# Kernel optimization log

Hardware: AMD Instinct MI355X
Metric: run time of the kernel (lower is better)

Reference implementation:

```python
import jax, jax.numpy as jnp
import numpy as np
from jax import lax

D = 1024  # inputSize == hidden size
B = 128   # batch
T = 256   # step


def setup_inputs() -> dict:
    key = jax.random.key(0)
    ks = jax.random.split(key, 9)
    s = 1.0 / np.sqrt(D)  # torch LSTMCell/Linear default init scale
    return {
        "inp": jax.random.normal(ks[0], (B, T, D), dtype=jnp.float32),
        "h0": jnp.zeros((B, D), dtype=jnp.float32),
        "c0": jnp.zeros((B, D), dtype=jnp.float32),
        "W_ih": jax.random.uniform(ks[1], (4 * D, D), jnp.float32, -s, s),
        "W_hh": jax.random.uniform(ks[2], (4 * D, D), jnp.float32, -s, s),
        "b_ih": jax.random.uniform(ks[3], (4 * D,), jnp.float32, -s, s),
        "b_hh": jax.random.uniform(ks[4], (4 * D,), jnp.float32, -s, s),
        "fc_w": jax.random.uniform(ks[5], (1, D), jnp.float32, -s, s),
        "fc_b": jax.random.uniform(ks[6], (1,), jnp.float32, -s, s),
        "step": T,
    }


def reference(inp, h0, c0, W_ih, W_hh, b_ih, b_hh, fc_w, fc_b, step):
    # The original's double python loop just transposes [B, T, D] -> [T, B, D].
    xs = jnp.swapaxes(inp, 0, 1)  # [T, B, D]

    def cell(carry, x):
        h, c = carry
        # torch.nn.LSTMCell gate order: i, f, g, o
        gates = x @ W_ih.T + b_ih + h @ W_hh.T + b_hh  # [B, 4D]
        i, f, g, o = jnp.split(gates, 4, axis=-1)
        i = jax.nn.sigmoid(i)
        f = jax.nn.sigmoid(f)
        g = jnp.tanh(g)
        o = jax.nn.sigmoid(o)
        c2 = f * c + i * g
        h2 = o * jnp.tanh(c2)
        return (h2, c2), None

    (hx, cx), _ = lax.scan(cell, (h0, c0), xs)
    yhat = jax.nn.sigmoid(hx @ fc_w.T + fc_b)  # [B, 1]
    return (yhat, hx, cx)
```

## Files before the change

### kernel.cpp

```cpp
#include <hip/hip_runtime.h>
#include <hip/hip_cooperative_groups.h>

namespace cg = cooperative_groups;

#define Dd 1024
#define Bb 128
#define Tt 256
#define NWG 256
#define NTHR 256

typedef short bf16x8 __attribute__((ext_vector_type(8)));
typedef float f32x4 __attribute__((ext_vector_type(4)));
typedef unsigned long long u64;

static __device__ __forceinline__ unsigned short f2bf(float x) {
  unsigned int u = __float_as_uint(x);
  u += 0x7fffu + ((u >> 16) & 1u);
  return (unsigned short)(u >> 16);
}
static __device__ __forceinline__ unsigned int pk2(float a, float b) {
  return (unsigned int)f2bf(a) | ((unsigned int)f2bf(b) << 16);
}
static __device__ __forceinline__ bf16x8 as_bf(uint4 u) {
  union { uint4 u; bf16x8 v; } x; x.u = u; return x.v;
}
static __device__ __forceinline__ f32x4 mfma_(bf16x8 a, bf16x8 b, f32x4 c) {
  return __builtin_amdgcn_mfma_f32_16x16x32_bf16(a, b, c, 0, 0, 0);
}
static __device__ __forceinline__ float sigm(float x) { return 1.f / (1.f + __expf(-x)); }
static __device__ __forceinline__ float tanh_s(float x) { return 1.f - 2.f / (__expf(2.f * x) + 1.f); }
static __device__ __forceinline__ u64 aload(const u64* p) {
  return __hip_atomic_load(p, __ATOMIC_RELAXED, __HIP_MEMORY_SCOPE_AGENT);
}
static __device__ __forceinline__ void astore(u64* p, u64 v) {
  __hip_atomic_store(p, v, __ATOMIC_RELAXED, __HIP_MEMORY_SCOPE_AGENT);
}

__global__ void __launch_bounds__(NTHR, 1) lstm_kernel(
    const float* __restrict__ inp, const float* __restrict__ h0,
    const float* __restrict__ c0, const float* __restrict__ W_ih,
    const float* __restrict__ W_hh, const float* __restrict__ b_ih,
    const float* __restrict__ b_hh, const float* __restrict__ fc_w,
    const float* __restrict__ fc_b, float* __restrict__ out,
    int* __restrict__ flags, unsigned short* __restrict__ hbuf,
    unsigned short* __restrict__ xbf, int use_xbf)
{
  extern __shared__ uint4 ldsW[];
  __shared__ float red[4];

  const int tid = threadIdx.x;
  const int wg  = blockIdx.x;
  const int gid = wg * NTHR + tid;
  cg::grid_group grid = cg::this_grid();

  const int gs = wg >> 1;
  const int bh = wg & 1;

  if (tid < 4)
    __hip_atomic_store(&flags[bh * 512 + gs * 4 + tid], 0,
                       __ATOMIC_RELAXED, __HIP_MEMORY_SCOPE_AGENT);

  if (use_xbf) {
    for (int i = gid; i < Tt * Bb * (Dd / 8); i += NWG * NTHR) {
      int d8 = i & 127, b = (i >> 7) & 127, t = i >> 14;
      const float* s = inp + ((size_t)b * Tt + t) * Dd + d8 * 8;
      uint4 p;
      p.x = pk2(s[0], s[1]); p.y = pk2(s[2], s[3]);
      p.z = pk2(s[4], s[5]); p.w = pk2(s[6], s[7]);
      *(uint4*)(xbf + (size_t)i * 8) = p;
    }
  }
  uint4* hb4w = (uint4*)hbuf;
  for (int i = gid; i < 128 * 128; i += NWG * NTHR) {
    int row = i & 127, gsl = i >> 7;
    const float* s = h0 + (size_t)row * Dd + gsl * 8;
    uint4 p;
    p.x = pk2(s[0], s[1]); p.y = pk2(s[2], s[3]);
    p.z = pk2(s[4], s[5]); p.w = pk2(s[6], s[7]);
    hb4w[gsl * 128 + row] = p;
  }

  for (int i = tid; i < 8192; i += NTHR) {
    int l2 = i & 63, mmct = (i >> 6) & 3, kc = i >> 8;
    int cc = l2 & 15, ct = mmct & 1;
    int row = (((ct << 1) | (cc >> 3)) << 10) | (gs << 3) | (cc & 7);
    int k = kc * 32 + ((l2 >> 4) << 3);
    const float* s = ((mmct & 2) ? W_hh : W_ih) + (size_t)row * Dd + k;
    uint4 p;
    p.x = pk2(s[0], s[1]); p.y = pk2(s[2], s[3]);
    p.z = pk2(s[4], s[5]); p.w = pk2(s[6], s[7]);
    ldsW[i] = p;
  }

  const int w = tid >> 6, l = tid & 63;
  const int c = l & 15;
  const int rowbase = bh * 64 + w * 16;
  const int arow = rowbase + c;
  const int koff8 = l >> 4;
  const int r0 = ((c >> 3) << 10) | (gs << 3) | (c & 7);
  const int r1 = ((2 + (c >> 3)) << 10) | (gs << 3) | (c & 7);
  const float bias0 = b_ih[r0] + b_hh[r0];
  const float bias1 = b_ih[r1] + b_hh[r1];
  const int dim = (gs << 3) | (c & 7);
  const int crow = rowbase + (koff8 << 2);
  float creg[4];
  #pragma unroll
  for (int j = 0; j < 4; ++j) creg[j] = c0[(size_t)(crow + j) * Dd + dim];

  float* out_y = out;
  float* out_h = out + Bb;
  float* out_c = out + Bb + (size_t)Bb * Dd;

  const u64* hQ = (const u64*)hbuf;
  int* myflag = &flags[bh * 512 + gs * 4 + w];
  const u64* fq = (const u64*)(flags + bh * 512);
  const int shbase = ((l & 15) >> 2) * 16;

  grid.sync();

  for (int t = 0; t < Tt; ++t) {
    const int cur = t & 1;
    f32x4 xa0 = {bias0, bias0, bias0, bias0};
    f32x4 xa1 = {bias1, bias1, bias1, bias1};
    f32x4 xb0 = {0.f, 0.f, 0.f, 0.f};
    f32x4 xb1 = {0.f, 0.f, 0.f, 0.f};

    if (use_xbf) {
      const uint4* xA = (const uint4*)(xbf + ((size_t)t * Bb + arow) * Dd + koff8 * 8);
      #pragma unroll
      for (int kc = 0; kc < 32; kc += 2) {
        uint4 ax0 = xA[kc * 4];
        uint4 ax1 = xA[(kc + 1) * 4];
        const int lb0 = kc * 256 + l, lb1 = (kc + 1) * 256 + l;
        xa0 = mfma_(as_bf(ax0), as_bf(ldsW[lb0]),      xa0);
        xa1 = mfma_(as_bf(ax0), as_bf(ldsW[lb0 + 64]), xa1);
        xb0 = mfma_(as_bf(ax1), as_bf(ldsW[lb1]),      xb0);
        xb1 = mfma_(as_bf(ax1), as_bf(ldsW[lb1 + 64]), xb1);
      }
    } else {
      const float* xF = inp + ((size_t)arow * Tt + t) * Dd + koff8 * 8;
      #pragma unroll 4
      for (int kc = 0; kc < 32; ++kc) {
        const float* xs = xF + kc * 32;
        uint4 axu;
        axu.x = pk2(xs[0], xs[1]); axu.y = pk2(xs[2], xs[3]);
        axu.z = pk2(xs[4], xs[5]); axu.w = pk2(xs[6], xs[7]);
        const int lb = kc * 256 + l;
        xa0 = mfma_(as_bf(axu), as_bf(ldsW[lb]),      xa0);
        xa1 = mfma_(as_bf(axu), as_bf(ldsW[lb + 64]), xa1);
      }
    }

    {
      int ok;
      do {
        u64 a = aload(&fq[l]);
        u64 b = aload(&fq[l + 64]);
        u64 c2 = aload(&fq[l + 128]);
        u64 d2 = aload(&fq[l + 192]);
        ok = ((int)a >= t) && ((int)(a >> 32) >= t) &&
             ((int)b >= t) && ((int)(b >> 32) >= t) &&
             ((int)c2 >= t) && ((int)(c2 >> 32) >= t) &&
             ((int)d2 >= t) && ((int)(d2 >> 32) >= t);
      } while (!__all(ok));
    }

    const u64* hA = hQ + (size_t)cur * 32768;
    #pragma unroll
    for (int kc = 0; kc < 32; kc += 2) {
      const int hi0 = (kc * 4 + koff8) * 256 + arow * 2;
      const int hi1 = ((kc + 1) * 4 + koff8) * 256 + arow * 2;
      union { u64 q[2]; uint4 p; } h0u, h1u;
      h0u.q[0] = aload(&hA[hi0]); h0u.q[1] = aload(&hA[hi0 + 1]);
      h1u.q[0] = aload(&hA[hi1]); h1u.q[1] = aload(&hA[hi1 + 1]);
      const int lb0 = kc * 256 + l, lb1 = (kc + 1) * 256 + l;
      xa0 = mfma_(as_bf(h0u.p), as_bf(ldsW[lb0 + 128]), xa0);
      xa1 = mfma_(as_bf(h0u.p), as_bf(ldsW[lb0 + 192]), xa1);
      xb0 = mfma_(as_bf(h1u.p), as_bf(ldsW[lb1 + 128]), xb0);
      xb1 = mfma_(as_bf(h1u.p), as_bf(ldsW[lb1 + 192]), xb1);
    }
    f32x4 acc0 = xa0 + xb0;
    f32x4 acc1 = xa1 + xb1;

    float fo0[4], fo1[4];
    #pragma unroll
    for (int j = 0; j < 4; ++j) {
      fo0[j] = __shfl_xor(acc0[j], 8);
      fo1[j] = __shfl_xor(acc1[j], 8);
    }
    unsigned int bfu0 = 0, bfu1 = 0, bfu2 = 0, bfu3 = 0;
    if (c < 8) {
      float hnv[4];
      #pragma unroll
      for (int j = 0; j < 4; ++j) {
        float iv = sigm(acc0[j]);
        float fv = sigm(fo0[j]);
        float gv = tanh_s(acc1[j]);
        float ov = sigm(fo1[j]);
        float cn = fv * creg[j] + iv * gv;
        float hn = ov * tanh_s(cn);
        creg[j] = cn;
        hnv[j] = hn;
        if (t == Tt - 1) {
          size_t off = (size_t)(crow + j) * Dd + dim;
          __hip_atomic_store(&out_h[off], hn, __ATOMIC_RELAXED, __HIP_MEMORY_SCOPE_AGENT);
          __hip_atomic_store(&out_c[off], cn, __ATOMIC_RELAXED, __HIP_MEMORY_SCOPE_AGENT);
        }
      }
      bfu0 = f2bf(hnv[0]); bfu1 = f2bf(hnv[1]);
      bfu2 = f2bf(hnv[2]); bfu3 = f2bf(hnv[3]);
    }

    unsigned int w0 = 0, w1 = 0, w2 = 0, w3 = 0;
    #pragma unroll
    for (int j = 0; j < 4; ++j) {
      unsigned int src = (j == 0) ? bfu0 : (j == 1) ? bfu1 : (j == 2) ? bfu2 : bfu3;
      unsigned int lo0 = __shfl((int)src, shbase + 0);
      unsigned int hi0g = __shfl((int)src, shbase + 1);
      unsigned int lo1 = __shfl((int)src, shbase + 2);
      unsigned int hi1g = __shfl((int)src, shbase + 3);
      unsigned int lo2 = __shfl((int)src, shbase + 4);
      unsigned int hi2g = __shfl((int)src, shbase + 5);
      unsigned int lo3 = __shfl((int)src, shbase + 6);
      unsigned int hi3g = __shfl((int)src, shbase + 7);
      bool mine = ((l & 3) == j);
      if (mine) {
        w0 = lo0 | (hi0g << 16);
        w1 = lo1 | (hi1g << 16);
        w2 = lo2 | (hi2g << 16);
        w3 = lo3 | (hi3g << 16);
      }
    }
    if (l < 16) {
      u64 q0 = (u64)w0 | ((u64)w1 << 32);
      u64 q1 = (u64)w2 | ((u64)w3 << 32);
      u64* hw = (u64*)(hbuf + (size_t)(cur ^ 1) * 131072
                       + (size_t)gs * 1024 + (size_t)(rowbase + l) * 8);
      astore(&hw[0], q0);
      astore(&hw[1], q1);
    }
    asm volatile("s_waitcnt vmcnt(0)" ::: "memory");
    if (l == 0)
      __hip_atomic_store(myflag, t + 1, __ATOMIC_RELAXED, __HIP_MEMORY_SCOPE_AGENT);
  }

  if (wg < Bb) {
    {
      const u64* fa = (const u64*)flags;
      int ok;
      do {
        ok = 1;
        #pragma unroll
        for (int r = 0; r < 8; ++r) {
          u64 v = aload(&fa[l + r * 64]);
          ok &= ((int)v >= Tt) && ((int)(v >> 32) >= Tt);
        }
      } while (!__all(ok));
    }
    const u64* hr = (const u64*)(out_h + (size_t)wg * Dd);
    float s = 0.f;
    for (int k = tid; k < Dd / 2; k += NTHR) {
      u64 v = aload(&hr[k]);
      union { u64 u; float f[2]; } q; q.u = v;
      s += q.f[0] * fc_w[2 * k] + q.f[1] * fc_w[2 * k + 1];
    }
    #pragma unroll
    for (int off = 32; off > 0; off >>= 1) s += __shfl_down(s, off);
    if (l == 0) red[w] = s;
    __syncthreads();
    if (tid == 0) {
      float tot = red[0] + red[1] + red[2] + red[3] + fc_b[0];
      out_y[wg] = sigm(tot);
    }
  }
}

extern "C" void kernel_launch(void* const* d_in, const int* in_sizes, int n_in,
                              void* d_out, int out_size, void* d_ws, size_t ws_size,
                              hipStream_t stream) {
  (void)in_sizes; (void)n_in; (void)out_size;
  const float* inp  = (const float*)d_in[0];
  const float* h0   = (const float*)d_in[1];
  const float* c0   = (const float*)d_in[2];
  const float* W_ih = (const float*)d_in[3];
  const float* W_hh = (const float*)d_in[4];
  const float* b_ih = (const float*)d_in[5];
  const float* b_hh = (const float*)d_in[6];
  const float* fc_w = (const float*)d_in[7];
  const float* fc_b = (const float*)d_in[8];
  float* out = (float*)d_out;

  size_t fbytes = 4096;
  size_t hbytes = (size_t)2 * Bb * Dd * 2;
  size_t xbytes = (size_t)Tt * Bb * Dd * 2;
  int* flags = (int*)d_ws;
  unsigned short* hbuf = (unsigned short*)((char*)d_ws + fbytes);
  unsigned short* xbf  = (unsigned short*)((char*)d_ws + fbytes + hbytes);
  int use_xbf = (ws_size >= fbytes + hbytes + xbytes) ? 1 : 0;

  hipFuncSetAttribute((const void*)lstm_kernel,
                      hipFuncAttributeMaxDynamicSharedMemorySize, 131072);

  void* kargs[] = {(void*)&inp, (void*)&h0, (void*)&c0, (void*)&W_ih, (void*)&W_hh,
                   (void*)&b_ih, (void*)&b_hh, (void*)&fc_w, (void*)&fc_b,
                   (void*)&out, (void*)&flags, (void*)&hbuf, (void*)&xbf, (void*)&use_xbf};
  hipLaunchCooperativeKernel((void*)lstm_kernel, dim3(NWG), dim3(NTHR),
                             kargs, 131072u, stream);
}
```

Measured before the change: 2.980 ms.

## Use per-step h ring buffer, single-wave flag polling, and plain vector h loads

Replaces the double-buffered h exchange with a ring holding one slot per timestep, so each slot is written once and can be read with ordinary non-atomic 128-bit loads without stale-cache hazards. Only wave 0 polls the global flags and then signals the other waves through an LDS variable, which cuts polling traffic. h stores use a cache-bypassing dwordx4 store. The ring costs T+1 slots of workspace, and the code falls back to the old path or drops the bf16 x precompute when the workspace is too small.

```diff
diff --git a/kernel.cpp b/kernel.cpp
--- a/kernel.cpp
+++ b/kernel.cpp
@@ -11,6 +11,7 @@
 
 typedef short bf16x8 __attribute__((ext_vector_type(8)));
 typedef float f32x4 __attribute__((ext_vector_type(4)));
+typedef unsigned int u32x4 __attribute__((ext_vector_type(4)));
 typedef unsigned long long u64;
 
 static __device__ __forceinline__ unsigned short f2bf(float x) {
@@ -32,10 +33,8 @@
 static __device__ __forceinline__ u64 aload(const u64* p) {
   return __hip_atomic_load(p, __ATOMIC_RELAXED, __HIP_MEMORY_SCOPE_AGENT);
 }
-static __device__ __forceinline__ void astore(u64* p, u64 v) {
-  __hip_atomic_store(p, v, __ATOMIC_RELAXED, __HIP_MEMORY_SCOPE_AGENT);
-}
-
+
+template<int RING>
 __global__ void __launch_bounds__(NTHR, 1) lstm_kernel(
     const float* __restrict__ inp, const float* __restrict__ h0,
     const float* __restrict__ c0, const float* __restrict__ W_ih,
@@ -47,6 +46,7 @@
 {
   extern __shared__ uint4 ldsW[];
   __shared__ float red[4];
+  __shared__ int sent;
 
   const int tid = threadIdx.x;
   const int wg  = blockIdx.x;
@@ -59,6 +59,7 @@
   if (tid < 4)
     __hip_atomic_store(&flags[bh * 512 + gs * 4 + tid], 0,
                        __ATOMIC_RELAXED, __HIP_MEMORY_SCOPE_AGENT);
+  if (tid == 0) sent = -1;
 
   if (use_xbf) {
     for (int i = gid; i < Tt * Bb * (Dd / 8); i += NWG * NTHR) {
@@ -111,7 +112,6 @@
   float* out_h = out + Bb;
   float* out_c = out + Bb + (size_t)Bb * Dd;
 
-  const u64* hQ = (const u64*)hbuf;
   int* myflag = &flags[bh * 512 + gs * 4 + w];
   const u64* fq = (const u64*)(flags + bh * 512);
   const int shbase = ((l & 15) >> 2) * 16;
@@ -119,7 +119,9 @@
   grid.sync();
 
   for (int t = 0; t < Tt; ++t) {
-    const int cur = t & 1;
+    const int rslot = RING ? t : (t & 1);
+    const int wslot = RING ? (t + 1) : ((t + 1) & 1);
+
     f32x4 xa0 = {bias0, bias0, bias0, bias0};
     f32x4 xa1 = {bias1, bias1, bias1, bias1};
     f32x4 xb0 = {0.f, 0.f, 0.f, 0.f};
@@ -151,7 +153,7 @@
       }
     }
 
-    {
+    if (w == 0) {
       int ok;
       do {
         u64 a = aload(&fq[l]);
@@ -163,21 +165,39 @@
              ((int)c2 >= t) && ((int)(c2 >> 32) >= t) &&
              ((int)d2 >= t) && ((int)(d2 >> 32) >= t);
       } while (!__all(ok));
-    }
-
-    const u64* hA = hQ + (size_t)cur * 32768;
-    #pragma unroll
-    for (int kc = 0; kc < 32; kc += 2) {
-      const int hi0 = (kc * 4 + koff8) * 256 + arow * 2;
-      const int hi1 = ((kc + 1) * 4 + koff8) * 256 + arow * 2;
-      union { u64 q[2]; uint4 p; } h0u, h1u;
-      h0u.q[0] = aload(&hA[hi0]); h0u.q[1] = aload(&hA[hi0 + 1]);
-      h1u.q[0] = aload(&hA[hi1]); h1u.q[1] = aload(&hA[hi1 + 1]);
-      const int lb0 = kc * 256 + l, lb1 = (kc + 1) * 256 + l;
-      xa0 = mfma_(as_bf(h0u.p), as_bf(ldsW[lb0 + 128]), xa0);
-      xa1 = mfma_(as_bf(h0u.p), as_bf(ldsW[lb0 + 192]), xa1);
-      xb0 = mfma_(as_bf(h1u.p), as_bf(ldsW[lb1 + 128]), xb0);
-      xb1 = mfma_(as_bf(h1u.p), as_bf(ldsW[lb1 + 192]), xb1);
+      __hip_atomic_store(&sent, t, __ATOMIC_RELEASE, __HIP_MEMORY_SCOPE_WORKGROUP);
+    } else {
+      while (__hip_atomic_load(&sent, __ATOMIC_ACQUIRE, __HIP_MEMORY_SCOPE_WORKGROUP) < t) {}
+    }
+    asm volatile("" ::: "memory");
+
+    if constexpr (RING) {
+      const uint4* hA4 = (const uint4*)(hbuf + (size_t)rslot * 131072);
+      #pragma unroll
+      for (int kc = 0; kc < 32; kc += 2) {
+        uint4 h0u = hA4[(kc * 4 + koff8) * 128 + arow];
+        uint4 h1u = hA4[((kc + 1) * 4 + koff8) * 128 + arow];
+        const int lb0 = kc * 256 + l, lb1 = (kc + 1) * 256 + l;
+        xa0 = mfma_(as_bf(h0u), as_bf(ldsW[lb0 + 128]), xa0);
+        xa1 = mfma_(as_bf(h0u), as_bf(ldsW[lb0 + 192]), xa1);
+        xb0 = mfma_(as_bf(h1u), as_bf(ldsW[lb1 + 128]), xb0);
+        xb1 = mfma_(as_bf(h1u), as_bf(ldsW[lb1 + 192]), xb1);
+      }
+    } else {
+      const u64* hA = (const u64*)hbuf + (size_t)rslot * 32768;
+      #pragma unroll
+      for (int kc = 0; kc < 32; kc += 2) {
+        const int hi0 = (kc * 4 + koff8) * 256 + arow * 2;
+        const int hi1 = ((kc + 1) * 4 + koff8) * 256 + arow * 2;
+        union { u64 q[2]; uint4 p4; } h0u, h1u;
+        h0u.q[0] = aload(&hA[hi0]); h0u.q[1] = aload(&hA[hi0 + 1]);
+        h1u.q[0] = aload(&hA[hi1]); h1u.q[1] = aload(&hA[hi1 + 1]);
+        const int lb0 = kc * 256 + l, lb1 = (kc + 1) * 256 + l;
+        xa0 = mfma_(as_bf(h0u.p4), as_bf(ldsW[lb0 + 128]), xa0);
+        xa1 = mfma_(as_bf(h0u.p4), as_bf(ldsW[lb0 + 192]), xa1);
+        xb0 = mfma_(as_bf(h1u.p4), as_bf(ldsW[lb1 + 128]), xb0);
+        xb1 = mfma_(as_bf(h1u.p4), as_bf(ldsW[lb1 + 192]), xb1);
+      }
     }
     f32x4 acc0 = xa0 + xb0;
     f32x4 acc1 = xa1 + xb1;
@@ -232,12 +252,11 @@
       }
     }
     if (l < 16) {
-      u64 q0 = (u64)w0 | ((u64)w1 << 32);
-      u64 q1 = (u64)w2 | ((u64)w3 << 32);
-      u64* hw = (u64*)(hbuf + (size_t)(cur ^ 1) * 131072
-                       + (size_t)gs * 1024 + (size_t)(rowbase + l) * 8);
-      astore(&hw[0], q0);
-      astore(&hw[1], q1);
+      u32x4 val = {w0, w1, w2, w3};
+      unsigned short* hw = hbuf + (size_t)wslot * 131072
+                           + (size_t)gs * 1024 + (size_t)(rowbase + l) * 8;
+      asm volatile("global_store_dwordx4 %0, %1, off sc0 sc1"
+                   :: "v"(hw), "v"(val) : "memory");
     }
     asm volatile("s_waitcnt vmcnt(0)" ::: "memory");
     if (l == 0)
@@ -290,20 +309,30 @@
   const float* fc_b = (const float*)d_in[8];
   float* out = (float*)d_out;
 
-  size_t fbytes = 4096;
-  size_t hbytes = (size_t)2 * Bb * Dd * 2;
-  size_t xbytes = (size_t)Tt * Bb * Dd * 2;
+  const size_t fbytes = 4096;
+  const size_t slot   = (size_t)Bb * Dd * 2;
+  const size_t ring1  = (size_t)(Tt + 1) * slot;
+  const size_t ring0  = 2 * slot;
+  const size_t xbytes = (size_t)Tt * Bb * Dd * 2;
+
+  int ring, use_xbf;
+  size_t rbytes;
+  if (ws_size >= fbytes + ring1 + xbytes)      { ring = 1; use_xbf = 1; rbytes = ring1; }
+  else if (ws_size >= fbytes + ring1)          { ring = 1; use_xbf = 0; rbytes = ring1; }
+  else if (ws_size >= fbytes + ring0 + xbytes) { ring = 0; use_xbf = 1; rbytes = ring0; }
+  else                                         { ring = 0; use_xbf = 0; rbytes = ring0; }
+
   int* flags = (int*)d_ws;
   unsigned short* hbuf = (unsigned short*)((char*)d_ws + fbytes);
-  unsigned short* xbf  = (unsigned short*)((char*)d_ws + fbytes + hbytes);
-  int use_xbf = (ws_size >= fbytes + hbytes + xbytes) ? 1 : 0;
-
-  hipFuncSetAttribute((const void*)lstm_kernel,
-                      hipFuncAttributeMaxDynamicSharedMemorySize, 131072);
+  unsigned short* xbf  = (unsigned short*)((char*)d_ws + fbytes + rbytes);
+
+  void* kfn = ring ? (void*)lstm_kernel<1> : (void*)lstm_kernel<0>;
+  (void)hipFuncSetAttribute((const void*)kfn,
+                            hipFuncAttributeMaxDynamicSharedMemorySize, 131072);
 
   void* kargs[] = {(void*)&inp, (void*)&h0, (void*)&c0, (void*)&W_ih, (void*)&W_hh,
                    (void*)&b_ih, (void*)&b_hh, (void*)&fc_w, (void*)&fc_b,
                    (void*)&out, (void*)&flags, (void*)&hbuf, (void*)&xbf, (void*)&use_xbf};
-  hipLaunchCooperativeKernel((void*)lstm_kernel, dim3(NWG), dim3(NTHR),
-                             kargs, 131072u, stream);
-}
+  (void)hipLaunchCooperativeKernel(kfn, dim3(NWG), dim3(NTHR),
+                                   kargs, 131072u, stream);
+}
```

After: 2.878 ms. -3.4%, faster.
